# Performance work log

Hardware: AMD Instinct MI355X
Metric: run time of the kernel (lower is better)

## Reference

```python
import jax, jax.numpy as jnp
import numpy as np

D_MODEL = 2048
N_EXPERTS = 8
TOP_K = 2
FFN_HIDDEN = int(D_MODEL * 1.5)  # 3072, matches int(d_model*1.5)


def setup_inputs() -> dict:
    key = jax.random.key(0)
    k_x, k_r, k_g, k_u, k_d = jax.random.split(key, 5)
    B, L = 4, 4096
    s_in = 1.0 / np.sqrt(D_MODEL)
    s_hid = 1.0 / np.sqrt(FFN_HIDDEN)
    return {
        "x": jax.random.normal(k_x, (B, L, D_MODEL), dtype=jnp.float32),
        # nn.Linear weights are stored (out_features, in_features)
        "router_w": jax.random.uniform(k_r, (N_EXPERTS, D_MODEL), jnp.float32, -s_in, s_in),
        "gate_w": jax.random.uniform(k_g, (N_EXPERTS, FFN_HIDDEN, D_MODEL), jnp.float32, -s_in, s_in),
        "up_w": jax.random.uniform(k_u, (N_EXPERTS, FFN_HIDDEN, D_MODEL), jnp.float32, -s_in, s_in),
        "down_w": jax.random.uniform(k_d, (N_EXPERTS, D_MODEL, FFN_HIDDEN), jnp.float32, -s_hid, s_hid),
    }


def reference(x, router_w, gate_w, up_w, down_w):
    B, L, D = x.shape
    x_flat = x.reshape(-1, D)                                   # [N, D]

    router_logits = x_flat @ router_w.T                          # [N, E]
    router_probs = jax.nn.softmax(router_logits, axis=-1)
    top_k_probs, top_k_idx = jax.lax.top_k(router_probs, TOP_K)  # [N, K]
    top_k_probs = top_k_probs / jnp.sum(top_k_probs, axis=-1, keepdims=True)

    # combine[n, e] = sum_k top_k_probs[n,k] * (top_k_idx[n,k] == e)
    onehot = jax.nn.one_hot(top_k_idx, N_EXPERTS, dtype=x.dtype)  # [N, K, E]
    combine = jnp.einsum("nk,nke->ne", top_k_probs, onehot)       # [N, E]

    # Masked gather/scatter in the original == weight-0 tokens here; same math.
    output = jnp.zeros_like(x_flat)
    for e in range(N_EXPERTS):
        gate = jax.nn.silu(x_flat @ gate_w[e].T)                  # [N, H]
        up = x_flat @ up_w[e].T                                   # [N, H]
        expert_out = (gate * up) @ down_w[e].T                    # [N, D]
        output = output + combine[:, e:e + 1] * expert_out

    # dropout is identity in eval/reference mode
    return output.reshape(B, L, D)
```

## Files before the change

### kernel.cpp

```cpp
#include <hip/hip_runtime.h>
#include <hip/hip_bf16.h>
#include <cstdint>

#define N_TOK 16384
#define DMODEL 2048
#define FFH    3072
#define NEXP   8
#define ATOT   32768

typedef __bf16 bf16;
typedef __attribute__((ext_vector_type(8))) __bf16 bf16x8;
typedef __attribute__((ext_vector_type(4))) __bf16 bf16x4;
typedef __attribute__((ext_vector_type(4))) float  f32x4;

__device__ __forceinline__ void gl_lds16(const bf16* g, void* l) {
  __builtin_amdgcn_global_load_lds(
      (const __attribute__((address_space(1))) void*)g,
      (__attribute__((address_space(3))) void*)l, 16, 0, 0);
}

__global__ void cvt_f32_bf16(const float* __restrict__ src, bf16* __restrict__ dst, long n4) {
  long i = (long)blockIdx.x * blockDim.x + threadIdx.x;
  if (i >= n4) return;
  const float4 v = ((const float4*)src)[i];
  bf16x4 o;
  o.x = (bf16)v.x; o.y = (bf16)v.y; o.z = (bf16)v.z; o.w = (bf16)v.w;
  ((bf16x4*)dst)[i] = o;
}

__global__ void router_k(const float* __restrict__ x, const float* __restrict__ rw,
                         int* __restrict__ tk_e, float* __restrict__ tk_w,
                         int* __restrict__ cnt) {
  const int wv = threadIdx.x >> 6, lane = threadIdx.x & 63;
  const int t = blockIdx.x * 4 + wv;
  const float* xr = x + (size_t)t * DMODEL;
  float acc[NEXP];
#pragma unroll
  for (int e = 0; e < NEXP; ++e) acc[e] = 0.f;
  for (int k = lane; k < DMODEL; k += 64) {
    const float xv = xr[k];
#pragma unroll
    for (int e = 0; e < NEXP; ++e) acc[e] = fmaf(xv, rw[e * DMODEL + k], acc[e]);
  }
#pragma unroll
  for (int e = 0; e < NEXP; ++e) {
#pragma unroll
    for (int o = 32; o; o >>= 1) acc[e] += __shfl_xor(acc[e], o, 64);
  }
  if (lane == 0) {
    int e0 = 0; float v0 = acc[0];
#pragma unroll
    for (int e = 1; e < NEXP; ++e) if (acc[e] > v0) { v0 = acc[e]; e0 = e; }
    int e1 = -1; float v1 = -1e30f;
#pragma unroll
    for (int e = 0; e < NEXP; ++e) if (e != e0 && acc[e] > v1) { v1 = acc[e]; e1 = e; }
    const float w0 = 1.f / (1.f + __expf(v1 - v0));
    tk_e[t * 2] = e0; tk_e[t * 2 + 1] = e1;
    tk_w[t * 2] = w0; tk_w[t * 2 + 1] = 1.f - w0;
    atomicAdd(&cnt[e0], 1); atomicAdd(&cnt[e1], 1);
  }
}

__global__ void offs_k(const int* __restrict__ cnt, int* __restrict__ offs) {
  if (threadIdx.x == 0) {
    int o = 0;
    for (int e = 0; e < NEXP; ++e) { offs[e] = o; o += cnt[e]; }
  }
}

__global__ void scatter_k(const int* __restrict__ tk_e, const float* __restrict__ tk_w,
                          const int* __restrict__ offs, int* __restrict__ cnt2,
                          int* __restrict__ tok_list, float* __restrict__ w_list) {
  const int t = blockIdx.x * 256 + threadIdx.x;
  if (t >= N_TOK) return;
#pragma unroll
  for (int k = 0; k < 2; ++k) {
    const int e = tk_e[t * 2 + k];
    const int p = atomicAdd(&cnt2[e], 1);
    tok_list[offs[e] + p] = t;
    w_list[offs[e] + p] = tk_w[t * 2 + k];
  }
}

__global__ __launch_bounds__(256, 2) void gemm_gu_k(
    const bf16* __restrict__ xb, const bf16* __restrict__ gw, const bf16* __restrict__ uw,
    bf16* __restrict__ hbuf, const int* __restrict__ tok_list,
    const int* __restrict__ cnt, const int* __restrict__ offs) {
  const int e = blockIdx.z;
  const int cn = cnt[e];
  const int mbase = blockIdx.y * 128;
  if (mbase >= cn) return;
  const int offE = offs[e];
  const int nbase = blockIdx.x * 128;

  __shared__ bf16 lA[128 * 32], lG[128 * 32], lU[128 * 32];

  const int tid = threadIdx.x;
  const int wv = tid >> 6, lane = tid & 63;
  const int wr = wv >> 1, wc = wv & 1;

  const int r0 = tid >> 2, r1 = r0 + 64;
  const int colel = (tid & 3) * 8;

  const int tok0 = tok_list[offE + min(mbase + r0, cn - 1)];
  const int tok1 = tok_list[offE + min(mbase + r1, cn - 1)];
  const bf16* gA0 = xb + (size_t)tok0 * DMODEL + colel;
  const bf16* gA1 = xb + (size_t)tok1 * DMODEL + colel;
  const bf16* gG0 = gw + ((size_t)e * FFH + nbase + r0) * DMODEL + colel;
  const bf16* gG1 = gw + ((size_t)e * FFH + nbase + r1) * DMODEL + colel;
  const bf16* gU0 = uw + ((size_t)e * FFH + nbase + r0) * DMODEL + colel;
  const bf16* gU1 = uw + ((size_t)e * FFH + nbase + r1) * DMODEL + colel;

  char* lAw = (char*)lA + wv * 1024;
  char* lGw = (char*)lG + wv * 1024;
  char* lUw = (char*)lU + wv * 1024;

  const f32x4 zero = {0.f, 0.f, 0.f, 0.f};
  f32x4 accG[4][4], accU[4][4];
#pragma unroll
  for (int i = 0; i < 4; ++i)
#pragma unroll
    for (int j = 0; j < 4; ++j) { accG[i][j] = zero; accU[i][j] = zero; }

  const int aoff = (wr * 64 + (lane & 15)) * 64 + (lane >> 4) * 16;
  const int boff = (wc * 64 + (lane & 15)) * 64 + (lane >> 4) * 16;

  for (int kk = 0; kk < DMODEL / 32; ++kk) {
    const int k0 = kk * 32;
    __syncthreads();
    gl_lds16(gA0 + k0, lAw);
    gl_lds16(gA1 + k0, lAw + 4096);
    gl_lds16(gG0 + k0, lGw);
    gl_lds16(gG1 + k0, lGw + 4096);
    gl_lds16(gU0 + k0, lUw);
    gl_lds16(gU1 + k0, lUw + 4096);
    __syncthreads();
    bf16x8 a[4], bg[4], bu[4];
#pragma unroll
    for (int i = 0; i < 4; ++i) {
      a[i]  = *(const bf16x8*)((const char*)lA + aoff + i * 16 * 64);
      bg[i] = *(const bf16x8*)((const char*)lG + boff + i * 16 * 64);
      bu[i] = *(const bf16x8*)((const char*)lU + boff + i * 16 * 64);
    }
#pragma unroll
    for (int mi = 0; mi < 4; ++mi)
#pragma unroll
      for (int ni = 0; ni < 4; ++ni) {
        accG[mi][ni] = __builtin_amdgcn_mfma_f32_16x16x32_bf16(a[mi], bg[ni], accG[mi][ni], 0, 0, 0);
        accU[mi][ni] = __builtin_amdgcn_mfma_f32_16x16x32_bf16(a[mi], bu[ni], accU[mi][ni], 0, 0, 0);
      }
  }

#pragma unroll
  for (int mi = 0; mi < 4; ++mi)
#pragma unroll
    for (int j = 0; j < 4; ++j) {
      const int mloc = wr * 64 + mi * 16 + (lane >> 4) * 4 + j;
      if (mbase + mloc < cn) {
        bf16* hr = hbuf + (size_t)(offE + mbase + mloc) * FFH + nbase + wc * 64 + (lane & 15);
#pragma unroll
        for (int ni = 0; ni < 4; ++ni) {
          const float g = accG[mi][ni][j], u = accU[mi][ni][j];
          hr[ni * 16] = (bf16)(g / (1.f + __expf(-g)) * u);
        }
      }
    }
}

__global__ __launch_bounds__(256, 2) void gemm_down_k(
    const bf16* __restrict__ hbuf, const bf16* __restrict__ dw, float* __restrict__ out,
    const int* __restrict__ tok_list, const float* __restrict__ w_list,
    const int* __restrict__ cnt, const int* __restrict__ offs) {
  const int e = blockIdx.z;
  const int cn = cnt[e];
  const int mbase = blockIdx.y * 128;
  if (mbase >= cn) return;
  const int offE = offs[e];
  const int nbase = blockIdx.x * 128;

  __shared__ bf16 lA[128 * 32], lB[128 * 32];

  const int tid = threadIdx.x;
  const int wv = tid >> 6, lane = tid & 63;
  const int wr = wv >> 1, wc = wv & 1;

  const int r0 = tid >> 2, r1 = r0 + 64;
  const int colel = (tid & 3) * 8;

  const bf16* gA0 = hbuf + (size_t)(offE + mbase + r0) * FFH + colel;
  const bf16* gA1 = hbuf + (size_t)(offE + mbase + r1) * FFH + colel;
  const bf16* gB0 = dw + ((size_t)e * DMODEL + nbase + r0) * FFH + colel;
  const bf16* gB1 = dw + ((size_t)e * DMODEL + nbase + r1) * FFH + colel;

  char* lAw = (char*)lA + wv * 1024;
  char* lBw = (char*)lB + wv * 1024;

  const f32x4 zero = {0.f, 0.f, 0.f, 0.f};
  f32x4 acc[4][4];
#pragma unroll
  for (int i = 0; i < 4; ++i)
#pragma unroll
    for (int j = 0; j < 4; ++j) acc[i][j] = zero;

  const int aoff = (wr * 64 + (lane & 15)) * 64 + (lane >> 4) * 16;
  const int boff = (wc * 64 + (lane & 15)) * 64 + (lane >> 4) * 16;

  for (int kk = 0; kk < FFH / 32; ++kk) {
    const int k0 = kk * 32;
    __syncthreads();
    gl_lds16(gA0 + k0, lAw);
    gl_lds16(gA1 + k0, lAw + 4096);
    gl_lds16(gB0 + k0, lBw);
    gl_lds16(gB1 + k0, lBw + 4096);
    __syncthreads();
    bf16x8 a[4], b[4];
#pragma unroll
    for (int i = 0; i < 4; ++i) {
      a[i] = *(const bf16x8*)((const char*)lA + aoff + i * 16 * 64);
      b[i] = *(const bf16x8*)((const char*)lB + boff + i * 16 * 64);
    }
#pragma unroll
    for (int mi = 0; mi < 4; ++mi)
#pragma unroll
      for (int ni = 0; ni < 4; ++ni)
        acc[mi][ni] = __builtin_amdgcn_mfma_f32_16x16x32_bf16(a[mi], b[ni], acc[mi][ni], 0, 0, 0);
  }

#pragma unroll
  for (int mi = 0; mi < 4; ++mi)
#pragma unroll
    for (int j = 0; j < 4; ++j) {
      const int mloc = wr * 64 + mi * 16 + (lane >> 4) * 4 + j;
      if (mbase + mloc < cn) {
        const int ar = offE + mbase + mloc;
        const int tok = tok_list[ar];
        const float wg = w_list[ar];
        float* orow = out + (size_t)tok * DMODEL + nbase + wc * 64 + (lane & 15);
#pragma unroll
        for (int ni = 0; ni < 4; ++ni)
          atomicAdd(&orow[ni * 16], wg * acc[mi][ni][j]);
      }
    }
}

extern "C" void kernel_launch(void* const* d_in, const int* in_sizes, int n_in,
                              void* d_out, int out_size, void* d_ws, size_t ws_size,
                              hipStream_t stream) {
  const float* x  = (const float*)d_in[0];
  const float* rw = (const float*)d_in[1];
  const float* gw = (const float*)d_in[2];
  const float* uw = (const float*)d_in[3];
  const float* dw = (const float*)d_in[4];
  float* out = (float*)d_out;

  char* ws = (char*)d_ws;
  size_t o = 0;
  auto alloc = [&](size_t bytes) {
    void* p = ws + o;
    o = (o + bytes + 255) & ~(size_t)255;
    return p;
  };

  bf16*  xb       = (bf16*)alloc((size_t)N_TOK * DMODEL * 2);
  bf16*  gwb      = (bf16*)alloc((size_t)NEXP * FFH * DMODEL * 2);
  bf16*  uwb      = (bf16*)alloc((size_t)NEXP * FFH * DMODEL * 2);
  bf16*  dwb      = (bf16*)alloc((size_t)NEXP * DMODEL * FFH * 2);
  bf16*  hbuf     = (bf16*)alloc((size_t)(ATOT + 128) * FFH * 2);
  int*   tok_list = (int*)alloc((ATOT + 128) * 4);
  float* w_list   = (float*)alloc((ATOT + 128) * 4);
  int*   tk_e     = (int*)alloc((size_t)N_TOK * 2 * 4);
  float* tk_w     = (float*)alloc((size_t)N_TOK * 2 * 4);
  int*   cnt      = (int*)alloc(64);
  int*   offs     = (int*)alloc(64);
  int*   cnt2     = (int*)alloc(64);

  hipMemsetAsync(cnt, 0, 64, stream);
  hipMemsetAsync(cnt2, 0, 64, stream);
  hipMemsetAsync(out, 0, (size_t)out_size * sizeof(float), stream);

  {
    long n4 = (long)N_TOK * DMODEL / 4;
    cvt_f32_bf16<<<(unsigned)((n4 + 255) / 256), 256, 0, stream>>>(x, xb, n4);
  }
  {
    long n4 = (long)NEXP * FFH * DMODEL / 4;
    cvt_f32_bf16<<<(unsigned)((n4 + 255) / 256), 256, 0, stream>>>(gw, gwb, n4);
    cvt_f32_bf16<<<(unsigned)((n4 + 255) / 256), 256, 0, stream>>>(uw, uwb, n4);
    cvt_f32_bf16<<<(unsigned)((n4 + 255) / 256), 256, 0, stream>>>(dw, dwb, n4);
  }

  router_k<<<N_TOK / 4, 256, 0, stream>>>(x, rw, tk_e, tk_w, cnt);
  offs_k<<<1, 64, 0, stream>>>(cnt, offs);
  scatter_k<<<N_TOK / 256, 256, 0, stream>>>(tk_e, tk_w, offs, cnt2, tok_list, w_list);

  gemm_gu_k<<<dim3(FFH / 128, ATOT / 128, NEXP), 256, 0, stream>>>(
      xb, gwb, uwb, hbuf, tok_list, cnt, offs);
  gemm_down_k<<<dim3(DMODEL / 128, ATOT / 128, NEXP), 256, 0, stream>>>(
      hbuf, dwb, out, tok_list, w_list, cnt, offs);
}
```

Before: 2.308 ms.

## Rewrite MoE GEMMs with 256x256 tiles, triple-buffered LDS, and atomic-free combine

Replaces the two expert GEMM kernels with one templated 512-thread kernel that uses 256x256 tiles, a three-stage LDS ring with prefetch two steps ahead, XOR-swizzled LDS layout, and raised MFMA priority. The gate and up weights are interleaved into a single B matrix in 32-row blocks so one accumulator set covers both. The down projection writes per-assignment rows to a buffer, and a separate combine kernel does the weighted sum, removing the fp32 atomics and the output memset. It aims to raise MFMA utilisation and cut LDS and global traffic, at the cost of higher register and LDS pressure, an extra fp32 intermediate buffer aliased with the weight buffer, and an extra kernel pass.

```diff
diff --git a/kernel.cpp b/kernel.cpp
--- a/kernel.cpp
+++ b/kernel.cpp
@@ -5,6 +5,7 @@
 #define N_TOK 16384
 #define DMODEL 2048
 #define FFH    3072
+#define NGU    (2 * FFH)
 #define NEXP   8
 #define ATOT   32768
 
@@ -28,6 +29,23 @@
   ((bf16x4*)dst)[i] = o;
 }
 
+__global__ void cvt_guw(const float* __restrict__ gw, const float* __restrict__ uw,
+                        bf16* __restrict__ guw) {
+  const long i = (long)blockIdx.x * 256 + threadIdx.x;
+  const int c8 = (int)(i & 255);
+  const long rg = i >> 8;
+  const int e = (int)(rg / NGU);
+  const int ri = (int)(rg - (long)e * NGU);
+  const int hb = ri >> 6, sub = ri & 63;
+  const float* src = (sub < 32 ? gw : uw) + ((size_t)e * FFH + hb * 32 + (sub & 31)) * DMODEL + c8 * 8;
+  const float4 v0 = ((const float4*)src)[0];
+  const float4 v1 = ((const float4*)src)[1];
+  bf16x8 o;
+  o[0] = (bf16)v0.x; o[1] = (bf16)v0.y; o[2] = (bf16)v0.z; o[3] = (bf16)v0.w;
+  o[4] = (bf16)v1.x; o[5] = (bf16)v1.y; o[6] = (bf16)v1.z; o[7] = (bf16)v1.w;
+  *(bf16x8*)(guw + rg * DMODEL + c8 * 8) = o;
+}
+
 __global__ void router_k(const float* __restrict__ x, const float* __restrict__ rw,
                          int* __restrict__ tk_e, float* __restrict__ tk_w,
                          int* __restrict__ cnt) {
@@ -70,177 +88,174 @@
 
 __global__ void scatter_k(const int* __restrict__ tk_e, const float* __restrict__ tk_w,
                           const int* __restrict__ offs, int* __restrict__ cnt2,
-                          int* __restrict__ tok_list, float* __restrict__ w_list) {
+                          int* __restrict__ tok_list, float* __restrict__ w_list,
+                          int* __restrict__ aidx) {
   const int t = blockIdx.x * 256 + threadIdx.x;
   if (t >= N_TOK) return;
 #pragma unroll
   for (int k = 0; k < 2; ++k) {
     const int e = tk_e[t * 2 + k];
     const int p = atomicAdd(&cnt2[e], 1);
-    tok_list[offs[e] + p] = t;
-    w_list[offs[e] + p] = tk_w[t * 2 + k];
-  }
-}
-
-__global__ __launch_bounds__(256, 2) void gemm_gu_k(
-    const bf16* __restrict__ xb, const bf16* __restrict__ gw, const bf16* __restrict__ uw,
-    bf16* __restrict__ hbuf, const int* __restrict__ tok_list,
-    const int* __restrict__ cnt, const int* __restrict__ offs) {
+    const int a = offs[e] + p;
+    tok_list[a] = t;
+    w_list[a] = tk_w[t * 2 + k];
+    aidx[t * 2 + k] = a;
+  }
+}
+
+template<int EPI>
+__global__ __launch_bounds__(512, 2) void gemm_moe(
+    const bf16* __restrict__ A, const bf16* __restrict__ B,
+    bf16* __restrict__ hbuf, float* __restrict__ ybuf,
+    const int* __restrict__ tok_list, const int* __restrict__ cnt,
+    const int* __restrict__ offs) {
+  constexpr int KD = EPI ? FFH : DMODEL;
+  constexpr int NT = KD / 32;
+  constexpr int BROWS = EPI ? DMODEL : NGU;
+
   const int e = blockIdx.z;
   const int cn = cnt[e];
-  const int mbase = blockIdx.y * 128;
+  const int mbase = blockIdx.y * 256;
   if (mbase >= cn) return;
   const int offE = offs[e];
-  const int nbase = blockIdx.x * 128;
-
-  __shared__ bf16 lA[128 * 32], lG[128 * 32], lU[128 * 32];
+  const int nbase = blockIdx.x * 256;
+
+  __shared__ char lds[98304];
+  char* const ldsA = lds;
+  char* const ldsB = lds + 49152;
 
   const int tid = threadIdx.x;
   const int wv = tid >> 6, lane = tid & 63;
-  const int wr = wv >> 1, wc = wv & 1;
-
-  const int r0 = tid >> 2, r1 = r0 + 64;
-  const int colel = (tid & 3) * 8;
-
-  const int tok0 = tok_list[offE + min(mbase + r0, cn - 1)];
-  const int tok1 = tok_list[offE + min(mbase + r1, cn - 1)];
-  const bf16* gA0 = xb + (size_t)tok0 * DMODEL + colel;
-  const bf16* gA1 = xb + (size_t)tok1 * DMODEL + colel;
-  const bf16* gG0 = gw + ((size_t)e * FFH + nbase + r0) * DMODEL + colel;
-  const bf16* gG1 = gw + ((size_t)e * FFH + nbase + r1) * DMODEL + colel;
-  const bf16* gU0 = uw + ((size_t)e * FFH + nbase + r0) * DMODEL + colel;
-  const bf16* gU1 = uw + ((size_t)e * FFH + nbase + r1) * DMODEL + colel;
-
-  char* lAw = (char*)lA + wv * 1024;
-  char* lGw = (char*)lG + wv * 1024;
-  char* lUw = (char*)lU + wv * 1024;
+  const int wr = wv >> 2, wc = wv & 3;
+
+  const int sr = tid >> 2;
+  const int swz8 = ((tid & 3) ^ (sr & 3)) * 8;
+  const bf16* pA[2]; const bf16* pB[2];
+  if (EPI == 0) {
+    const int t0 = tok_list[offE + min(mbase + sr, cn - 1)];
+    const int t1 = tok_list[offE + min(mbase + 128 + sr, cn - 1)];
+    pA[0] = A + (size_t)t0 * KD + swz8;
+    pA[1] = A + (size_t)t1 * KD + swz8;
+  } else {
+    const int a0 = offE + min(mbase + sr, cn - 1);
+    const int a1 = offE + min(mbase + 128 + sr, cn - 1);
+    pA[0] = A + (size_t)a0 * KD + swz8;
+    pA[1] = A + (size_t)a1 * KD + swz8;
+  }
+  pB[0] = B + ((size_t)e * BROWS + nbase + sr) * KD + swz8;
+  pB[1] = B + ((size_t)e * BROWS + nbase + 128 + sr) * KD + swz8;
+
+  const int stageDst = wv * 1024;
+
+  const int rswz = ((lane >> 4) ^ (lane & 3)) * 16;
+  const int arow = (wr * 128 + (lane & 15)) * 64 + rswz;
+  const int brow = (wc * 64 + (lane & 15)) * 64 + rswz;
 
   const f32x4 zero = {0.f, 0.f, 0.f, 0.f};
-  f32x4 accG[4][4], accU[4][4];
-#pragma unroll
-  for (int i = 0; i < 4; ++i)
-#pragma unroll
-    for (int j = 0; j < 4; ++j) { accG[i][j] = zero; accU[i][j] = zero; }
-
-  const int aoff = (wr * 64 + (lane & 15)) * 64 + (lane >> 4) * 16;
-  const int boff = (wc * 64 + (lane & 15)) * 64 + (lane >> 4) * 16;
-
-  for (int kk = 0; kk < DMODEL / 32; ++kk) {
-    const int k0 = kk * 32;
-    __syncthreads();
-    gl_lds16(gA0 + k0, lAw);
-    gl_lds16(gA1 + k0, lAw + 4096);
-    gl_lds16(gG0 + k0, lGw);
-    gl_lds16(gG1 + k0, lGw + 4096);
-    gl_lds16(gU0 + k0, lUw);
-    gl_lds16(gU1 + k0, lUw + 4096);
-    __syncthreads();
-    bf16x8 a[4], bg[4], bu[4];
-#pragma unroll
-    for (int i = 0; i < 4; ++i) {
-      a[i]  = *(const bf16x8*)((const char*)lA + aoff + i * 16 * 64);
-      bg[i] = *(const bf16x8*)((const char*)lG + boff + i * 16 * 64);
-      bu[i] = *(const bf16x8*)((const char*)lU + boff + i * 16 * 64);
+  f32x4 acc[8][4];
+#pragma unroll
+  for (int i = 0; i < 8; ++i)
+#pragma unroll
+    for (int j = 0; j < 4; ++j) acc[i][j] = zero;
+
+  auto stage_half = [&](int buf, int q, int kt) {
+    const int k8 = kt * 32;
+    if (q < 2) gl_lds16(pA[q] + k8, ldsA + buf * 16384 + q * 8192 + stageDst);
+    else       gl_lds16(pB[q - 2] + k8, ldsB + buf * 16384 + (q - 2) * 8192 + stageDst);
+  };
+
+#pragma unroll
+  for (int q = 0; q < 4; ++q) stage_half(0, q, 0);
+#pragma unroll
+  for (int q = 0; q < 4; ++q) stage_half(1, q, 1);
+  asm volatile("s_waitcnt vmcnt(4)" ::: "memory");
+  __builtin_amdgcn_s_barrier();
+  asm volatile("" ::: "memory");
+
+  int cb = 0;
+  for (int kt = 0; kt < NT; ++kt) {
+    const int sb = (cb + 2 >= 3) ? cb - 1 : cb + 2;
+    const char* cA = ldsA + cb * 16384;
+    const char* cB = ldsB + cb * 16384;
+    bf16x8 bfr[4];
+#pragma unroll
+    for (int q = 0; q < 4; ++q) {
+      const bf16x8 a0 = *(const bf16x8*)(cA + (q * 2) * 1024 + arow);
+      const bf16x8 a1 = *(const bf16x8*)(cA + (q * 2 + 1) * 1024 + arow);
+      if (q == 0) {
+#pragma unroll
+        for (int nf = 0; nf < 4; ++nf)
+          bfr[nf] = *(const bf16x8*)(cB + nf * 1024 + brow);
+      }
+      if (kt + 2 < NT) stage_half(sb, q, kt + 2);
+      asm volatile("" ::: "memory");
+      __builtin_amdgcn_s_barrier();
+      asm volatile("" ::: "memory");
+      __builtin_amdgcn_s_setprio(1);
+#pragma unroll
+      for (int nf = 0; nf < 4; ++nf) {
+        acc[q * 2][nf]     = __builtin_amdgcn_mfma_f32_16x16x32_bf16(a0, bfr[nf], acc[q * 2][nf], 0, 0, 0);
+        acc[q * 2 + 1][nf] = __builtin_amdgcn_mfma_f32_16x16x32_bf16(a1, bfr[nf], acc[q * 2 + 1][nf], 0, 0, 0);
+      }
+      __builtin_amdgcn_s_setprio(0);
+      if (q == 3) {
+        if (kt + 2 < NT) { asm volatile("s_waitcnt vmcnt(4)" ::: "memory"); }
+        else             { asm volatile("s_waitcnt vmcnt(0)" ::: "memory"); }
+      }
+      asm volatile("" ::: "memory");
+      __builtin_amdgcn_s_barrier();
+      asm volatile("" ::: "memory");
     }
-#pragma unroll
-    for (int mi = 0; mi < 4; ++mi)
-#pragma unroll
-      for (int ni = 0; ni < 4; ++ni) {
-        accG[mi][ni] = __builtin_amdgcn_mfma_f32_16x16x32_bf16(a[mi], bg[ni], accG[mi][ni], 0, 0, 0);
-        accU[mi][ni] = __builtin_amdgcn_mfma_f32_16x16x32_bf16(a[mi], bu[ni], accU[mi][ni], 0, 0, 0);
-      }
-  }
-
-#pragma unroll
-  for (int mi = 0; mi < 4; ++mi)
-#pragma unroll
-    for (int j = 0; j < 4; ++j) {
-      const int mloc = wr * 64 + mi * 16 + (lane >> 4) * 4 + j;
-      if (mbase + mloc < cn) {
-        bf16* hr = hbuf + (size_t)(offE + mbase + mloc) * FFH + nbase + wc * 64 + (lane & 15);
-#pragma unroll
-        for (int ni = 0; ni < 4; ++ni) {
-          const float g = accG[mi][ni][j], u = accU[mi][ni][j];
-          hr[ni * 16] = (bf16)(g / (1.f + __expf(-g)) * u);
+    cb = (cb + 1 == 3) ? 0 : cb + 1;
+  }
+
+  const int col = lane & 15;
+  const int rb = mbase + wr * 128 + (lane >> 4) * 4;
+  if (EPI == 0) {
+    const int hb32 = ((nbase + wc * 64) >> 6) * 32;
+#pragma unroll
+    for (int mi = 0; mi < 8; ++mi)
+#pragma unroll
+      for (int j = 0; j < 4; ++j) {
+        const int row = rb + mi * 16 + j;
+        if (row < cn) {
+          bf16* hr = hbuf + (size_t)(offE + row) * FFH + hb32 + col;
+#pragma unroll
+          for (int k = 0; k < 2; ++k) {
+            const float g = acc[mi][k][j], u = acc[mi][k + 2][j];
+            hr[k * 16] = (bf16)(g / (1.f + __expf(-g)) * u);
+          }
         }
       }
-    }
-}
-
-__global__ __launch_bounds__(256, 2) void gemm_down_k(
-    const bf16* __restrict__ hbuf, const bf16* __restrict__ dw, float* __restrict__ out,
-    const int* __restrict__ tok_list, const float* __restrict__ w_list,
-    const int* __restrict__ cnt, const int* __restrict__ offs) {
-  const int e = blockIdx.z;
-  const int cn = cnt[e];
-  const int mbase = blockIdx.y * 128;
-  if (mbase >= cn) return;
-  const int offE = offs[e];
-  const int nbase = blockIdx.x * 128;
-
-  __shared__ bf16 lA[128 * 32], lB[128 * 32];
-
-  const int tid = threadIdx.x;
-  const int wv = tid >> 6, lane = tid & 63;
-  const int wr = wv >> 1, wc = wv & 1;
-
-  const int r0 = tid >> 2, r1 = r0 + 64;
-  const int colel = (tid & 3) * 8;
-
-  const bf16* gA0 = hbuf + (size_t)(offE + mbase + r0) * FFH + colel;
-  const bf16* gA1 = hbuf + (size_t)(offE + mbase + r1) * FFH + colel;
-  const bf16* gB0 = dw + ((size_t)e * DMODEL + nbase + r0) * FFH + colel;
-  const bf16* gB1 = dw + ((size_t)e * DMODEL + nbase + r1) * FFH + colel;
-
-  char* lAw = (char*)lA + wv * 1024;
-  char* lBw = (char*)lB + wv * 1024;
-
-  const f32x4 zero = {0.f, 0.f, 0.f, 0.f};
-  f32x4 acc[4][4];
-#pragma unroll
-  for (int i = 0; i < 4; ++i)
-#pragma unroll
-    for (int j = 0; j < 4; ++j) acc[i][j] = zero;
-
-  const int aoff = (wr * 64 + (lane & 15)) * 64 + (lane >> 4) * 16;
-  const int boff = (wc * 64 + (lane & 15)) * 64 + (lane >> 4) * 16;
-
-  for (int kk = 0; kk < FFH / 32; ++kk) {
-    const int k0 = kk * 32;
-    __syncthreads();
-    gl_lds16(gA0 + k0, lAw);
-    gl_lds16(gA1 + k0, lAw + 4096);
-    gl_lds16(gB0 + k0, lBw);
-    gl_lds16(gB1 + k0, lBw + 4096);
-    __syncthreads();
-    bf16x8 a[4], b[4];
-#pragma unroll
-    for (int i = 0; i < 4; ++i) {
-      a[i] = *(const bf16x8*)((const char*)lA + aoff + i * 16 * 64);
-      b[i] = *(const bf16x8*)((const char*)lB + boff + i * 16 * 64);
-    }
-#pragma unroll
-    for (int mi = 0; mi < 4; ++mi)
-#pragma unroll
-      for (int ni = 0; ni < 4; ++ni)
-        acc[mi][ni] = __builtin_amdgcn_mfma_f32_16x16x32_bf16(a[mi], b[ni], acc[mi][ni], 0, 0, 0);
-  }
-
-#pragma unroll
-  for (int mi = 0; mi < 4; ++mi)
-#pragma unroll
-    for (int j = 0; j < 4; ++j) {
-      const int mloc = wr * 64 + mi * 16 + (lane >> 4) * 4 + j;
-      if (mbase + mloc < cn) {
-        const int ar = offE + mbase + mloc;
-        const int tok = tok_list[ar];
-        const float wg = w_list[ar];
-        float* orow = out + (size_t)tok * DMODEL + nbase + wc * 64 + (lane & 15);
-#pragma unroll
-        for (int ni = 0; ni < 4; ++ni)
-          atomicAdd(&orow[ni * 16], wg * acc[mi][ni][j]);
-      }
-    }
+  } else {
+#pragma unroll
+    for (int mi = 0; mi < 8; ++mi)
+#pragma unroll
+      for (int j = 0; j < 4; ++j) {
+        const int row = rb + mi * 16 + j;
+        if (row < cn) {
+          float* yr = ybuf + (size_t)(offE + row) * DMODEL + nbase + wc * 64 + col;
+#pragma unroll
+          for (int nf = 0; nf < 4; ++nf) yr[nf * 16] = acc[mi][nf][j];
+        }
+      }
+  }
+}
+
+__global__ void combine_k(const float* __restrict__ ybuf, const int* __restrict__ aidx,
+                          const float* __restrict__ tk_w, float* __restrict__ out) {
+  const int i = blockIdx.x * 256 + threadIdx.x;
+  const int t = i >> 9, c = i & 511;
+  const int a0 = aidx[t * 2], a1 = aidx[t * 2 + 1];
+  const float w0 = tk_w[t * 2], w1 = tk_w[t * 2 + 1];
+  const float4 v0 = ((const float4*)(ybuf + (size_t)a0 * DMODEL))[c];
+  const float4 v1 = ((const float4*)(ybuf + (size_t)a1 * DMODEL))[c];
+  float4 o;
+  o.x = w0 * v0.x + w1 * v1.x;
+  o.y = w0 * v0.y + w1 * v1.y;
+  o.z = w0 * v0.z + w1 * v1.z;
+  o.w = w0 * v0.w + w1 * v1.w;
+  ((float4*)(out + (size_t)t * DMODEL))[c] = o;
 }
 
 extern "C" void kernel_launch(void* const* d_in, const int* in_sizes, int n_in,
@@ -261,40 +276,44 @@
     return p;
   };
 
+  const size_t guw_bytes  = (size_t)NEXP * NGU * DMODEL * 2;
+  const size_t ybuf_bytes = (size_t)(ATOT + 256) * DMODEL * 4;
   bf16*  xb       = (bf16*)alloc((size_t)N_TOK * DMODEL * 2);
-  bf16*  gwb      = (bf16*)alloc((size_t)NEXP * FFH * DMODEL * 2);
-  bf16*  uwb      = (bf16*)alloc((size_t)NEXP * FFH * DMODEL * 2);
+  void*  uni      = alloc(ybuf_bytes > guw_bytes ? ybuf_bytes : guw_bytes);
+  bf16*  guw      = (bf16*)uni;
+  float* ybuf     = (float*)uni;
   bf16*  dwb      = (bf16*)alloc((size_t)NEXP * DMODEL * FFH * 2);
-  bf16*  hbuf     = (bf16*)alloc((size_t)(ATOT + 128) * FFH * 2);
-  int*   tok_list = (int*)alloc((ATOT + 128) * 4);
-  float* w_list   = (float*)alloc((ATOT + 128) * 4);
+  bf16*  hbuf     = (bf16*)alloc((size_t)(ATOT + 256) * FFH * 2);
+  int*   tok_list = (int*)alloc((ATOT + 256) * 4);
+  float* w_list   = (float*)alloc((ATOT + 256) * 4);
   int*   tk_e     = (int*)alloc((size_t)N_TOK * 2 * 4);
   float* tk_w     = (float*)alloc((size_t)N_TOK * 2 * 4);
+  int*   aidx     = (int*)alloc((size_t)N_TOK * 2 * 4);
   int*   cnt      = (int*)alloc(64);
   int*   offs     = (int*)alloc(64);
   int*   cnt2     = (int*)alloc(64);
 
   hipMemsetAsync(cnt, 0, 64, stream);
   hipMemsetAsync(cnt2, 0, 64, stream);
-  hipMemsetAsync(out, 0, (size_t)out_size * sizeof(float), stream);
 
   {
     long n4 = (long)N_TOK * DMODEL / 4;
-    cvt_f32_bf16<<<(unsigned)((n4 + 255) / 256), 256, 0, stream>>>(x, xb, n4);
-  }
+    cvt_f32_bf16<<<(unsigned)(n4 / 256), 256, 0, stream>>>(x, xb, n4);
+  }
+  cvt_guw<<<(unsigned)((long)NEXP * NGU * DMODEL / 8 / 256), 256, 0, stream>>>(gw, uw, guw);
   {
-    long n4 = (long)NEXP * FFH * DMODEL / 4;
-    cvt_f32_bf16<<<(unsigned)((n4 + 255) / 256), 256, 0, stream>>>(gw, gwb, n4);
-    cvt_f32_bf16<<<(unsigned)((n4 + 255) / 256), 256, 0, stream>>>(uw, uwb, n4);
-    cvt_f32_bf16<<<(unsigned)((n4 + 255) / 256), 256, 0, stream>>>(dw, dwb, n4);
+    long n4 = (long)NEXP * DMODEL * FFH / 4;
+    cvt_f32_bf16<<<(unsigned)(n4 / 256), 256, 0, stream>>>(dw, dwb, n4);
   }
 
   router_k<<<N_TOK / 4, 256, 0, stream>>>(x, rw, tk_e, tk_w, cnt);
   offs_k<<<1, 64, 0, stream>>>(cnt, offs);
-  scatter_k<<<N_TOK / 256, 256, 0, stream>>>(tk_e, tk_w, offs, cnt2, tok_list, w_list);
-
-  gemm_gu_k<<<dim3(FFH / 128, ATOT / 128, NEXP), 256, 0, stream>>>(
-      xb, gwb, uwb, hbuf, tok_list, cnt, offs);
-  gemm_down_k<<<dim3(DMODEL / 128, ATOT / 128, NEXP), 256, 0, stream>>>(
-      hbuf, dwb, out, tok_list, w_list, cnt, offs);
-}
+  scatter_k<<<N_TOK / 256, 256, 0, stream>>>(tk_e, tk_w, offs, cnt2, tok_list, w_list, aidx);
+
+  gemm_moe<0><<<dim3(NGU / 256, 64, NEXP), 512, 0, stream>>>(
+      xb, guw, hbuf, nullptr, tok_list, cnt, offs);
+  gemm_moe<1><<<dim3(DMODEL / 256, 64, NEXP), 512, 0, stream>>>(
+      hbuf, dwb, nullptr, ybuf, tok_list, cnt, offs);
+
+  combine_k<<<N_TOK * 512 / 256, 256, 0, stream>>>(ybuf, aidx, tk_w, out);
+}
```

New measurement: 2.123 ms. -8.0%, faster.
